# Kernel optimization log

Hardware: AMD Instinct MI355X
Metric: run time of the kernel (lower is better)

Reference implementation:

```python
import jax, jax.numpy as jnp
import numpy as np

B, N_VEC, D, C, N_W, N_CLASS, VOCAB = 16, 4096, 256, 256, 12, 10, 32
N_LINKS = N_W + 1


def _chord_cols(n_vec, n_links):
    # cols[i] = [i, (i+2^0)%n, (i+2^1)%n, ..., (i+2^(L-2))%n]
    i = np.arange(n_vec)[:, None]
    offs = np.concatenate([[0], 2 ** np.arange(n_links - 1)])[None, :]
    return ((i + offs) % n_vec).astype(np.int32)


def setup_inputs() -> dict:
    key = jax.random.key(0)
    ks = jax.random.split(key, 16)
    s = 0.02
    return {
        "tokens": jax.random.randint(ks[0], (B, N_VEC), 0, VOCAB),
        "cols": jnp.asarray(_chord_cols(N_VEC, N_LINKS)),
        "emb": jax.random.normal(ks[1], (VOCAB, D), jnp.float32) * s,
        "pos_emb": jax.random.normal(ks[2], (N_VEC, D), jnp.float32) * s,
        "g_w1": jax.random.normal(ks[3], (D, C), jnp.float32) * s,
        "g_b1": jnp.zeros((C,), jnp.float32),
        "g_w2": jax.random.normal(ks[4], (C, C), jnp.float32) * s,
        "g_b2": jnp.zeros((C,), jnp.float32),
        "fs_w1": jax.random.normal(ks[5], (N_W, D, D), jnp.float32) * s,
        "fs_b1": jnp.zeros((N_W, D), jnp.float32),
        "fs_w2": jax.random.normal(ks[6], (N_W, D, N_LINKS), jnp.float32) * s,
        "fs_b2": jnp.zeros((N_W, N_LINKS), jnp.float32),
        "fin_w": jax.random.normal(ks[7], (C, N_CLASS), jnp.float32) * s,
        "fin_b": jnp.zeros((N_CLASS,), jnp.float32),
    }


def reference(tokens, cols, emb, pos_emb, g_w1, g_b1, g_w2, g_b2,
              fs_w1, fs_b1, fs_w2, fs_b2, fin_w, fin_b):
    # token + positional embedding: [B, N, D]
    data = emb[tokens] + pos_emb[None, :, :]
    # g MLP -> V: [B, N, C]   (torch GELU = exact erf)
    V = jax.nn.gelu(data @ g_w1 + g_b1, approximate=False) @ g_w2 + g_b2
    res = V
    n_w = fs_w1.shape[0]
    for m in range(n_w):
        # per-edge weights: [B, N, L]
        W = jax.nn.gelu(data @ fs_w1[m] + fs_b1[m], approximate=False) @ fs_w2[m] + fs_b2[m]
        # chord spmm: V[b,i] = sum_l W[b,i,l] * V[b, cols[i,l]]
        Vg = V[:, cols, :]                       # [B, N, L, C]
        V = jnp.einsum('bnl,bnlc->bnc', W, Vg) + res
    cls = V[:, 0, :]                             # CLS pooling
    return cls @ fin_w + fin_b
```

## Files before the change

kernel.cpp:

```cpp
#include <hip/hip_runtime.h>
#include <hip/hip_bf16.h>
#include <math.h>

namespace {

constexpr int Bb   = 16;
constexpr int Nv   = 4096;
constexpr int NW   = 12;
constexpr int NL   = 13;
constexpr int NCLS = 10;
constexpr int BN   = Bb * Nv;

typedef __attribute__((ext_vector_type(8))) short short8;
typedef __attribute__((ext_vector_type(4))) float float4_t;

__device__ __forceinline__ float gelu_poly(float x) {
    float u = x * x;
    float p = fmaf(u, fmaf(u, fmaf(u, -2.374656431e-3f, 1.994711402e-2f),
                           -1.329807601e-1f), 7.978845608e-1f);
    return x * fmaf(x * p, 0.5f, 0.5f);
}
__device__ __forceinline__ float bflo(unsigned int u) {
    return __builtin_bit_cast(float, u << 16);
}
__device__ __forceinline__ float bfhi(unsigned int u) {
    return __builtin_bit_cast(float, u & 0xffff0000u);
}
__device__ __forceinline__ unsigned int f2bf(float f) {
    unsigned int x = __builtin_bit_cast(unsigned int, f);
    x += 0x7fff + ((x >> 16) & 1);
    return x >> 16;
}
__device__ __forceinline__ unsigned short f2bf16(float f) {
    return __builtin_bit_cast(unsigned short, __float2bfloat16(f));
}
__device__ __forceinline__ void gload16(const unsigned short* g, unsigned short* l) {
    __builtin_amdgcn_global_load_lds(
        (const __attribute__((address_space(1))) void*)g,
        (__attribute__((address_space(3))) void*)l, 16, 0, 0);
}
__device__ __forceinline__ int xcd_swz(int bid) {
    return (bid & 7) * 128 + (bid >> 3);
}


__global__ __launch_bounds__(256) void xbf_kernel(
    const int* __restrict__ tokens,
    const float* __restrict__ emb,
    const float* __restrict__ pos,
    unsigned int* __restrict__ Xbf)
{
    int i  = blockIdx.x * 256 + threadIdx.x;
    int p  = i & 127;
    int bn = i >> 7;
    int n  = bn & (Nv - 1);
    int t  = tokens[bn];
    const float2* e2 = (const float2*)(emb + (size_t)t * 256);
    const float2* p2 = (const float2*)(pos + (size_t)n * 256);
    float2 a = e2[p], b = p2[p];
    Xbf[i] = f2bf(a.x + b.x) | (f2bf(a.y + b.y) << 16);
}

__global__ __launch_bounds__(256) void wt_kernel(
    const float* __restrict__ g_w1,
    const float* __restrict__ g_w2,
    const float* __restrict__ fs_w1,
    const float* __restrict__ fs_w2,
    unsigned short* __restrict__ WT,
    unsigned short* __restrict__ W2T)
{
    int bid = blockIdx.x;
    int t = threadIdx.x;
    if (bid < 14 * 16) {
        int mat = bid >> 4;
        int k0  = (bid & 15) * 16;
        const float* src = (mat == 0) ? g_w1
                         : (mat == 1) ? g_w2
                         : fs_w1 + (size_t)(mat - 2) * 65536;
        unsigned short tmp[16];
#pragma unroll
        for (int j = 0; j < 16; ++j)
            tmp[j] = (unsigned short)f2bf(src[(size_t)(k0 + j) * 256 + t]);
        unsigned short* dst = WT + ((size_t)mat * 256 + t) * 256 + k0;
#pragma unroll
        for (int j = 0; j < 16; ++j) dst[j] = tmp[j];
    } else {
        int m = bid - 224;
        const float* src = fs_w2 + (size_t)m * 256 * NL;
        unsigned short* dst = W2T + (size_t)m * 4096;
#pragma unroll
        for (int i = 0; i < 16; ++i) {
            int idx = t + i * 256;
            int n = idx >> 8, k = idx & 255;
            dst[idx] = (n < NL) ? (unsigned short)f2bf(src[(size_t)k * NL + n]) : 0;
        }
    }
}


__device__ __forceinline__ void stage32(
    const unsigned short* __restrict__ Xg,
    const unsigned short* __restrict__ Wg,
    int row0, int k0, int tid,
    unsigned short* Xs, unsigned short* Ws)
{
    {
        int slot = tid;
        int row = slot >> 2, pu = slot & 3, lu = pu ^ (row & 3);
        gload16(Xg + (size_t)(row0 + row) * 256 + k0 + lu * 8, Xs + slot * 8);
    }
#pragma unroll
    for (int i = 0; i < 2; ++i) {
        int slot = i * 512 + tid;
        int n = slot >> 2, pu = slot & 3, lu = pu ^ (n & 3);
        gload16(Wg + (size_t)n * 256 + k0 + lu * 8, Ws + slot * 8);
    }
}

__device__ __forceinline__ void compute32(
    const unsigned short* Xs, const unsigned short* Ws,
    int wr, int wc, int l15, int lg, float4_t acc[4][4])
{
    short8 a[4], b[4];
#pragma unroll
    for (int fr = 0; fr < 4; ++fr) {
        int r = wr * 64 + fr * 16 + l15;
        a[fr] = *(const short8*)(Xs + r * 32 + ((lg ^ (r & 3)) << 3));
    }
#pragma unroll
    for (int nt = 0; nt < 4; ++nt) {
        int n = wc * 64 + nt * 16 + l15;
        b[nt] = *(const short8*)(Ws + n * 32 + ((lg ^ (n & 3)) << 3));
    }
#pragma unroll
    for (int fr = 0; fr < 4; ++fr)
#pragma unroll
        for (int nt = 0; nt < 4; ++nt)
            acc[fr][nt] = __builtin_amdgcn_mfma_f32_16x16x32_bf16(
                a[fr], b[nt], acc[fr][nt], 0, 0, 0);
}

__device__ __forceinline__ void gemm_2ph(
    const unsigned short* __restrict__ Xg,
    const unsigned short* __restrict__ Wg,
    int row0, int tid,
    unsigned short* Xs0, unsigned short* Ws0,
    unsigned short* Xs1, unsigned short* Ws1,
    float4_t acc[4][4])
{
    const int w = tid >> 6, lane = tid & 63;
    const int wr = w >> 2, wc = w & 3;
    const int l15 = lane & 15, lg = lane >> 4;
    (void)w;

    stage32(Xg, Wg, row0, 0, tid, Xs0, Ws0);
    __syncthreads();
#pragma unroll
    for (int t = 0; t < 8; ++t) {
        unsigned short* Xc = (t & 1) ? Xs1 : Xs0;
        unsigned short* Wc = (t & 1) ? Ws1 : Ws0;
        unsigned short* Xn = (t & 1) ? Xs0 : Xs1;
        unsigned short* Wn = (t & 1) ? Ws0 : Ws1;
        if (t < 7) stage32(Xg, Wg, row0, (t + 1) * 32, tid, Xn, Wn);
        compute32(Xc, Wc, wr, wc, l15, lg, acc);
        __syncthreads();
    }
}

template<bool GELU>
__global__ __launch_bounds__(512) void gemm_act_kernel(
    const unsigned short* __restrict__ X,
    const unsigned short* __restrict__ WT,
    const float* __restrict__ bias,
    unsigned short* __restrict__ Y)
{
    __shared__ __align__(128) unsigned char smem[49152];
    unsigned short* Xs0 = (unsigned short*)smem;
    unsigned short* Ws0 = (unsigned short*)(smem + 8192);
    unsigned short* Xs1 = (unsigned short*)(smem + 24576);
    unsigned short* Ws1 = (unsigned short*)(smem + 32768);

    const int row0 = ((blockIdx.x & 7) * 64 + (blockIdx.x >> 3)) * 128;
    const int tid  = threadIdx.x;
    const int w = tid >> 6, lane = tid & 63;
    const int wr = w >> 2, wc = w & 3;
    const int l15 = lane & 15, lg = lane >> 4;

    float4_t acc[4][4];
#pragma unroll
    for (int fr = 0; fr < 4; ++fr)
#pragma unroll
        for (int nt = 0; nt < 4; ++nt) acc[fr][nt] = (float4_t)0.f;

    gemm_2ph(X, WT, row0, tid, Xs0, Ws0, Xs1, Ws1, acc);

#pragma unroll
    for (int nt = 0; nt < 4; ++nt) {
        int c = wc * 64 + nt * 16 + l15;
        float bv = bias[c];
#pragma unroll
        for (int fr = 0; fr < 4; ++fr)
#pragma unroll
            for (int reg = 0; reg < 4; ++reg) {
                float v = acc[fr][nt][reg] + bv;
                if (GELU) v = gelu_poly(v);
                Y[(size_t)(row0 + wr * 64 + fr * 16 + lg * 4 + reg) * 256 + c]
                    = f2bf16(v);
            }
    }
}

__global__ __launch_bounds__(512) void fsmlp_kernel(
    const unsigned short* __restrict__ X,
    const unsigned short* __restrict__ WT,
    const unsigned short* __restrict__ W2T,
    const float* __restrict__ fs_b1,
    const float* __restrict__ fs_b2,
    float* __restrict__ Wall)
{
    __shared__ __align__(128) unsigned char smem[65536];
    unsigned short* Xs0 = (unsigned short*)smem;
    unsigned short* Ws0 = (unsigned short*)(smem + 8192);
    unsigned short* Xs1 = (unsigned short*)(smem + 24576);
    unsigned short* Ws1 = (unsigned short*)(smem + 32768);
    unsigned short* Hs  = (unsigned short*)smem;

    const int bid  = (blockIdx.x & 7) * 768 + (blockIdx.x >> 3);
    const int m    = bid % 12;
    const int row0 = (bid / 12) * 128;
    const int tid  = threadIdx.x;
    const int w = tid >> 6, lane = tid & 63;
    const int wr = w >> 2, wc = w & 3;
    const int l15 = lane & 15, lg = lane >> 4;

    const unsigned short* Wg   = WT + (size_t)(2 + m) * 65536;
    const unsigned short* W2Tm = W2T + (size_t)m * 4096;
    const float* b1m = fs_b1 + (size_t)m * 256;
    const float* b2m = fs_b2 + (size_t)m * NL;
    float* Wallm = Wall + (size_t)m * BN * NL;

    float4_t acc[4][4];
#pragma unroll
    for (int fr = 0; fr < 4; ++fr)
#pragma unroll
        for (int nt = 0; nt < 4; ++nt) acc[fr][nt] = (float4_t)0.f;

    gemm_2ph(X, Wg, row0, tid, Xs0, Ws0, Xs1, Ws1, acc);

    short8 b2[8];
#pragma unroll
    for (int kc = 0; kc < 8; ++kc)
        b2[kc] = *(const short8*)(W2Tm + l15 * 256 + kc * 32 + lg * 8);

#pragma unroll
    for (int nt = 0; nt < 4; ++nt) {
        int c = wc * 64 + nt * 16 + l15;
        float bv = b1m[c];
        int cu = c >> 3, cl = c & 7;
#pragma unroll
        for (int fr = 0; fr < 4; ++fr)
#pragma unroll
            for (int reg = 0; reg < 4; ++reg) {
                int row = wr * 64 + fr * 16 + lg * 4 + reg;
                Hs[row * 256 + ((cu ^ (row & 7)) << 3) + cl] =
                    f2bf16(gelu_poly(acc[fr][nt][reg] + bv));
            }
    }
    __syncthreads();

    float4_t wacc = (float4_t)0.f;
#pragma unroll
    for (int kc = 0; kc < 8; ++kc) {
        int ua = (((kc * 4 + lg) ^ (l15 & 7)) << 3);
        short8 a = *(const short8*)(Hs + (w * 16 + l15) * 256 + ua);
        wacc = __builtin_amdgcn_mfma_f32_16x16x32_bf16(a, b2[kc], wacc, 0, 0, 0);
    }
    if (l15 < NL) {
        float b2v = b2m[l15];
#pragma unroll
        for (int reg = 0; reg < 4; ++reg)
            Wallm[(size_t)(row0 + w * 16 + lg * 4 + reg) * NL + l15]
                = wacc[reg] + b2v;
    }
}

__global__ __launch_bounds__(256) void chord_kernel(
    const unsigned short* __restrict__ Vprev,
    const uint2* __restrict__ res,
    const float* __restrict__ Wm,
    uint2* __restrict__ Vnext)
{
    __shared__ __align__(16) unsigned short Vs[96 * 256];
    __shared__ float Wmix[64][NL];

    const int bid  = xcd_swz(blockIdx.x);
    const int row0 = bid * 64;
    const int n0   = row0 & (Nv - 1);
    const int bb   = row0 & ~(Nv - 1);
    const int tid  = threadIdx.x;

    for (int e = tid; e < 64 * NL; e += 256)
        Wmix[0][e] = Wm[(size_t)row0 * NL + e];

#pragma unroll
    for (int i = 0; i < 12; ++i) {
        int slot = i * 256 + tid;
        int j = slot >> 5, cu = slot & 31;
        int gr = bb + ((n0 + j) & (Nv - 1));
        gload16(Vprev + (size_t)gr * 256 + cu * 8, Vs + slot * 8);
    }
    __syncthreads();

    const int p = tid & 63;
    const int w = tid >> 6;
    const uint2* V2 = (const uint2*)Vprev;

    for (int it = 0; it < 16; ++it) {
        const int r = w * 16 + it;
        const size_t rb = (size_t)(row0 + r) * 64;
        uint2 rv = res[rb + p];
        float a0 = bflo(rv.x), a1 = bfhi(rv.x);
        float a2 = bflo(rv.y), a3 = bfhi(rv.y);

        const unsigned short* lbase = Vs + r * 256 + p * 4;
#pragma unroll
        for (int l = 0; l < 7; ++l) {
            const int off = (l == 0) ? 0 : (1 << (l - 1));
            uint2 gv = *(const uint2*)(lbase + off * 256);
            float wv = Wmix[r][l];
            a0 += wv * bflo(gv.x);  a1 += wv * bfhi(gv.x);
            a2 += wv * bflo(gv.y);  a3 += wv * bfhi(gv.y);
        }
#pragma unroll
        for (int l = 7; l < NL; ++l) {
            const int off = 1 << (l - 1);
            int gr = bb + ((n0 + r + off) & (Nv - 1));
            uint2 gv = V2[(size_t)gr * 64 + p];
            float wv = Wmix[r][l];
            a0 += wv * bflo(gv.x);  a1 += wv * bfhi(gv.x);
            a2 += wv * bflo(gv.y);  a3 += wv * bfhi(gv.y);
        }
        uint2 o;
        o.x = f2bf(a0) | (f2bf(a1) << 16);
        o.y = f2bf(a2) | (f2bf(a3) << 16);
        Vnext[rb + p] = o;
    }
}

__global__ __launch_bounds__(256) void final_kernel(
    const unsigned short* __restrict__ Vfin,
    const float* __restrict__ fin_w,
    const float* __restrict__ fin_b,
    float* __restrict__ out)
{
    int t = threadIdx.x;
    if (t < Bb * NCLS) {
        int b = t / NCLS, o = t % NCLS;
        float a = fin_b[o];
        const unsigned short* v = Vfin + (size_t)b * Nv * 256;
        for (int k = 0; k < 256; ++k)
            a += __builtin_bit_cast(float, (unsigned int)v[k] << 16)
                 * fin_w[k * NCLS + o];
        out[t] = a;
    }
}

}

extern "C" void kernel_launch(void* const* d_in, const int* in_sizes, int n_in,
                              void* d_out, int out_size, void* d_ws, size_t ws_size,
                              hipStream_t stream) {
    const int*   tokens = (const int*)d_in[0];
    const float* emb    = (const float*)d_in[2];
    const float* pos    = (const float*)d_in[3];
    const float* g_w1   = (const float*)d_in[4];
    const float* g_b1   = (const float*)d_in[5];
    const float* g_w2   = (const float*)d_in[6];
    const float* g_b2   = (const float*)d_in[7];
    const float* fs_w1  = (const float*)d_in[8];
    const float* fs_b1  = (const float*)d_in[9];
    const float* fs_w2  = (const float*)d_in[10];
    const float* fs_b2  = (const float*)d_in[11];
    const float* fin_w  = (const float*)d_in[12];
    const float* fin_b  = (const float*)d_in[13];
    float* out = (float*)d_out;

    unsigned short* Xbf = (unsigned short*)d_ws;
    unsigned short* WT  = Xbf + (size_t)BN * 256;
    unsigned short* W2T = WT + (size_t)14 * 65536;
    unsigned short* res = W2T + (size_t)12 * 4096;
    unsigned short* Va  = res + (size_t)BN * 256;
    unsigned short* Vb  = Va + (size_t)BN * 256;
    float* Wall = (float*)(Vb + (size_t)BN * 256);

    xbf_kernel<<<BN * 128 / 256, 256, 0, stream>>>(tokens, emb, pos,
                                                   (unsigned int*)Xbf);
    wt_kernel<<<14 * 16 + 12, 256, 0, stream>>>(g_w1, g_w2, fs_w1, fs_w2,
                                                WT, W2T);

    gemm_act_kernel<true><<<512, 512, 0, stream>>>(Xbf, WT, g_b1, Va);
    gemm_act_kernel<false><<<512, 512, 0, stream>>>(Va, WT + 65536, g_b2, res);

    fsmlp_kernel<<<6144, 512, 0, stream>>>(Xbf, WT, W2T, fs_b1, fs_b2, Wall);

    const unsigned short* vp = res;
    for (int m = 0; m < NW; ++m) {
        unsigned short* vn = (m & 1) ? Vb : Va;
        chord_kernel<<<1024, 256, 0, stream>>>(
            vp, (const uint2*)res,
            Wall + (size_t)m * BN * NL, (uint2*)vn);
        vp = vn;
    }

    final_kernel<<<1, 256, 0, stream>>>(vp, fin_w, fin_b, out);
}
```

Measured before the change: 596.1 us.

## Software-pipeline chord gathers and change LDS swizzle in GEMM tiles

The chord kernel now prefetches the far-offset global gathers and residual for the next row into registers while computing the current row, double-buffering across two register sets and overlapping with the shared-memory staging before the barrier. The GEMM LDS swizzle changes from XOR on row&3 to (row>>1)&3 to alter bank-conflict patterns for the MFMA fragment reads. The prefetching raises register pressure in the chord kernel, and the new swizzle may or may not reduce LDS conflicts.

After: 594.5 us. Within noise of the previous version (-0.3%).

```diff
diff --git a/kernel.cpp b/kernel.cpp
--- a/kernel.cpp
+++ b/kernel.cpp
@@ -106,13 +106,13 @@
 {
     {
         int slot = tid;
-        int row = slot >> 2, pu = slot & 3, lu = pu ^ (row & 3);
+        int row = slot >> 2, pu = slot & 3, lu = pu ^ ((row >> 1) & 3);
         gload16(Xg + (size_t)(row0 + row) * 256 + k0 + lu * 8, Xs + slot * 8);
     }
 #pragma unroll
     for (int i = 0; i < 2; ++i) {
         int slot = i * 512 + tid;
-        int n = slot >> 2, pu = slot & 3, lu = pu ^ (n & 3);
+        int n = slot >> 2, pu = slot & 3, lu = pu ^ ((n >> 1) & 3);
         gload16(Wg + (size_t)n * 256 + k0 + lu * 8, Ws + slot * 8);
     }
 }
@@ -125,12 +125,12 @@
 #pragma unroll
     for (int fr = 0; fr < 4; ++fr) {
         int r = wr * 64 + fr * 16 + l15;
-        a[fr] = *(const short8*)(Xs + r * 32 + ((lg ^ (r & 3)) << 3));
+        a[fr] = *(const short8*)(Xs + r * 32 + ((lg ^ ((r >> 1) & 3)) << 3));
     }
 #pragma unroll
     for (int nt = 0; nt < 4; ++nt) {
         int n = wc * 64 + nt * 16 + l15;
-        b[nt] = *(const short8*)(Ws + n * 32 + ((lg ^ (n & 3)) << 3));
+        b[nt] = *(const short8*)(Ws + n * 32 + ((lg ^ ((n >> 1) & 3)) << 3));
     }
 #pragma unroll
     for (int fr = 0; fr < 4; ++fr)
@@ -151,7 +151,6 @@
     const int w = tid >> 6, lane = tid & 63;
     const int wr = w >> 2, wc = w & 3;
     const int l15 = lane & 15, lg = lane >> 4;
-    (void)w;
 
     stage32(Xg, Wg, row0, 0, tid, Xs0, Ws0);
     __syncthreads();
@@ -284,6 +283,43 @@
     }
 }
 
+#define CHORD_PREF(FARR, RREG, RN)                                            \
+    {   const int rn_ = (RN);                                                 \
+        RREG = res[(size_t)(row0 + rn_) * 64 + p];                            \
+        _Pragma("unroll")                                                     \
+        for (int l = 7; l < NL; ++l) {                                        \
+            const int off = 1 << (l - 1);                                     \
+            FARR[l - 7] =                                                     \
+                V2[(size_t)(bb + ((n0 + rn_ + off) & (Nv - 1))) * 64 + p];    \
+        }                                                                     \
+    }
+
+#define CHORD_BODY(FARR, RREG, R)                                             \
+    {   const int r_ = (R);                                                   \
+        float a0 = bflo(RREG.x), a1 = bfhi(RREG.x);                           \
+        float a2 = bflo(RREG.y), a3 = bfhi(RREG.y);                           \
+        const unsigned short* lbase = Vs + r_ * 256 + p * 4;                  \
+        _Pragma("unroll")                                                     \
+        for (int l = 0; l < 7; ++l) {                                         \
+            const int off = (l == 0) ? 0 : (1 << (l - 1));                    \
+            uint2 gv = *(const uint2*)(lbase + off * 256);                    \
+            float wv = Wmix[r_][l];                                           \
+            a0 += wv * bflo(gv.x);  a1 += wv * bfhi(gv.x);                    \
+            a2 += wv * bflo(gv.y);  a3 += wv * bfhi(gv.y);                    \
+        }                                                                     \
+        _Pragma("unroll")                                                     \
+        for (int l = 7; l < NL; ++l) {                                        \
+            uint2 gv = FARR[l - 7];                                           \
+            float wv = Wmix[r_][l];                                           \
+            a0 += wv * bflo(gv.x);  a1 += wv * bfhi(gv.x);                    \
+            a2 += wv * bflo(gv.y);  a3 += wv * bfhi(gv.y);                    \
+        }                                                                     \
+        uint2 o;                                                              \
+        o.x = f2bf(a0) | (f2bf(a1) << 16);                                    \
+        o.y = f2bf(a2) | (f2bf(a3) << 16);                                    \
+        Vnext[(size_t)(row0 + r_) * 64 + p] = o;                              \
+    }
+
 __global__ __launch_bounds__(256) void chord_kernel(
     const unsigned short* __restrict__ Vprev,
     const uint2* __restrict__ res,
@@ -309,41 +345,23 @@
         int gr = bb + ((n0 + j) & (Nv - 1));
         gload16(Vprev + (size_t)gr * 256 + cu * 8, Vs + slot * 8);
     }
-    __syncthreads();
 
     const int p = tid & 63;
     const int w = tid >> 6;
     const uint2* V2 = (const uint2*)Vprev;
 
-    for (int it = 0; it < 16; ++it) {
-        const int r = w * 16 + it;
-        const size_t rb = (size_t)(row0 + r) * 64;
-        uint2 rv = res[rb + p];
-        float a0 = bflo(rv.x), a1 = bfhi(rv.x);
-        float a2 = bflo(rv.y), a3 = bfhi(rv.y);
-
-        const unsigned short* lbase = Vs + r * 256 + p * 4;
-#pragma unroll
-        for (int l = 0; l < 7; ++l) {
-            const int off = (l == 0) ? 0 : (1 << (l - 1));
-            uint2 gv = *(const uint2*)(lbase + off * 256);
-            float wv = Wmix[r][l];
-            a0 += wv * bflo(gv.x);  a1 += wv * bfhi(gv.x);
-            a2 += wv * bflo(gv.y);  a3 += wv * bfhi(gv.y);
-        }
-#pragma unroll
-        for (int l = 7; l < NL; ++l) {
-            const int off = 1 << (l - 1);
-            int gr = bb + ((n0 + r + off) & (Nv - 1));
-            uint2 gv = V2[(size_t)gr * 64 + p];
-            float wv = Wmix[r][l];
-            a0 += wv * bflo(gv.x);  a1 += wv * bfhi(gv.x);
-            a2 += wv * bflo(gv.y);  a3 += wv * bfhi(gv.y);
-        }
-        uint2 o;
-        o.x = f2bf(a0) | (f2bf(a1) << 16);
-        o.y = f2bf(a2) | (f2bf(a3) << 16);
-        Vnext[rb + p] = o;
+    uint2 fA[6], fB[6];
+    uint2 rA, rB;
+    CHORD_PREF(fA, rA, w * 16);
+    __syncthreads();
+
+#pragma unroll
+    for (int it2 = 0; it2 < 8; ++it2) {
+        const int r = w * 16 + it2 * 2;
+        CHORD_PREF(fB, rB, r + 1);
+        CHORD_BODY(fA, rA, r);
+        if (it2 < 7) CHORD_PREF(fA, rA, r + 2);
+        CHORD_BODY(fB, rB, r + 1);
     }
 }
 
```

## Use single-buffered 64-wide K tiles in first GEMM and retune LDS swizzle

Applied to the files above, without the earlier changes.

The standalone gemm_act_kernel now uses a new core that stages 64-wide K slices (4 iterations instead of 8) into a single LDS buffer with an 8-way XOR swizzle, halving the number of barrier-separated steps. It gives up the double-buffered prefetch overlap, so global loads no longer overlap MFMA work within a block. The shared 32-wide staging path (still used by other kernels) changes its swizzle from row&3 to (row>>1)&3 to reduce LDS bank conflicts on the ds_read pattern.

After: 570.3 us (median of 3 runs). -4.3%, faster.

```diff
diff --git a/kernel.cpp b/kernel.cpp
--- a/kernel.cpp
+++ b/kernel.cpp
@@ -97,6 +97,60 @@
     }
 }
 
+__device__ __forceinline__ void gemm1_core(
+    const unsigned short* __restrict__ Xg,
+    const unsigned short* __restrict__ Wg,
+    int row0, int tid,
+    unsigned short* Xs,
+    unsigned short* Wls,
+    float4_t acc[4][4])
+{
+    const int w = tid >> 6, lane = tid & 63;
+    const int wr = w >> 2, wc = w & 3;
+    const int l15 = lane & 15, lg = lane >> 4;
+
+    for (int k0 = 0; k0 < 256; k0 += 64) {
+#pragma unroll
+        for (int i = 0; i < 2; ++i) {
+            int slotb = i * 512 + w * 64;
+            int slot = slotb + lane;
+            int row = slot >> 3, pu = slot & 7, lu = pu ^ (row & 7);
+            gload16(Xg + (size_t)(row0 + row) * 256 + k0 + lu * 8, Xs + slotb * 8);
+        }
+#pragma unroll
+        for (int i = 0; i < 4; ++i) {
+            int slotb = i * 512 + w * 64;
+            int slot = slotb + lane;
+            int n = slot >> 3, pu = slot & 7, lu = pu ^ (n & 7);
+            gload16(Wg + (size_t)n * 256 + k0 + lu * 8, Wls + slotb * 8);
+        }
+        __syncthreads();
+
+#pragma unroll
+        for (int ks = 0; ks < 2; ++ks) {
+            short8 a[4], b[4];
+#pragma unroll
+            for (int fr = 0; fr < 4; ++fr) {
+                int r = wr * 64 + fr * 16 + l15;
+                int off = r * 128 + (((lg + ks * 4) ^ (l15 & 7)) << 4);
+                a[fr] = *(const short8*)((const char*)Xs + off);
+            }
+#pragma unroll
+            for (int nt = 0; nt < 4; ++nt) {
+                int n = wc * 64 + nt * 16 + l15;
+                int off = n * 128 + (((lg + ks * 4) ^ (l15 & 7)) << 4);
+                b[nt] = *(const short8*)((const char*)Wls + off);
+            }
+#pragma unroll
+            for (int fr = 0; fr < 4; ++fr)
+#pragma unroll
+                for (int nt = 0; nt < 4; ++nt)
+                    acc[fr][nt] = __builtin_amdgcn_mfma_f32_16x16x32_bf16(
+                        a[fr], b[nt], acc[fr][nt], 0, 0, 0);
+        }
+        __syncthreads();
+    }
+}
 
 __device__ __forceinline__ void stage32(
     const unsigned short* __restrict__ Xg,
@@ -106,13 +160,13 @@
 {
     {
         int slot = tid;
-        int row = slot >> 2, pu = slot & 3, lu = pu ^ (row & 3);
+        int row = slot >> 2, pu = slot & 3, lu = pu ^ ((row >> 1) & 3);
         gload16(Xg + (size_t)(row0 + row) * 256 + k0 + lu * 8, Xs + slot * 8);
     }
 #pragma unroll
     for (int i = 0; i < 2; ++i) {
         int slot = i * 512 + tid;
-        int n = slot >> 2, pu = slot & 3, lu = pu ^ (n & 3);
+        int n = slot >> 2, pu = slot & 3, lu = pu ^ ((n >> 1) & 3);
         gload16(Wg + (size_t)n * 256 + k0 + lu * 8, Ws + slot * 8);
     }
 }
@@ -125,12 +179,12 @@
 #pragma unroll
     for (int fr = 0; fr < 4; ++fr) {
         int r = wr * 64 + fr * 16 + l15;
-        a[fr] = *(const short8*)(Xs + r * 32 + ((lg ^ (r & 3)) << 3));
+        a[fr] = *(const short8*)(Xs + r * 32 + ((lg ^ ((r >> 1) & 3)) << 3));
     }
 #pragma unroll
     for (int nt = 0; nt < 4; ++nt) {
         int n = wc * 64 + nt * 16 + l15;
-        b[nt] = *(const short8*)(Ws + n * 32 + ((lg ^ (n & 3)) << 3));
+        b[nt] = *(const short8*)(Ws + n * 32 + ((lg ^ ((n >> 1) & 3)) << 3));
     }
 #pragma unroll
     for (int fr = 0; fr < 4; ++fr)
@@ -151,7 +205,6 @@
     const int w = tid >> 6, lane = tid & 63;
     const int wr = w >> 2, wc = w & 3;
     const int l15 = lane & 15, lg = lane >> 4;
-    (void)w;
 
     stage32(Xg, Wg, row0, 0, tid, Xs0, Ws0);
     __syncthreads();
@@ -175,10 +228,8 @@
     unsigned short* __restrict__ Y)
 {
     __shared__ __align__(128) unsigned char smem[49152];
-    unsigned short* Xs0 = (unsigned short*)smem;
-    unsigned short* Ws0 = (unsigned short*)(smem + 8192);
-    unsigned short* Xs1 = (unsigned short*)(smem + 24576);
-    unsigned short* Ws1 = (unsigned short*)(smem + 32768);
+    unsigned short* Xs  = (unsigned short*)smem;
+    unsigned short* Wls = (unsigned short*)(smem + 16384);
 
     const int row0 = ((blockIdx.x & 7) * 64 + (blockIdx.x >> 3)) * 128;
     const int tid  = threadIdx.x;
@@ -192,7 +243,7 @@
 #pragma unroll
         for (int nt = 0; nt < 4; ++nt) acc[fr][nt] = (float4_t)0.f;
 
-    gemm_2ph(X, WT, row0, tid, Xs0, Ws0, Xs1, Ws1, acc);
+    gemm1_core(X, WT, row0, tid, Xs, Wls, acc);
 
 #pragma unroll
     for (int nt = 0; nt < 4; ++nt) {
```
